# Performance work log

Hardware: AMD Instinct MI355X
Metric: run time of the kernel (lower is better)

The kernel has to match this reference:

```python
import jax, jax.numpy as jnp
import numpy as np

N, E, G, H = 5000, 50000, 8, 4
GAT_DIMS = [(1536, 1024), (1024, 512), (512, 256)]
MLP_DIMS = [(256, 128), (128, 64), (64, 32), (32, 16), (16, 1)]
GATE_DIMS = [(256, 128), (128, 1)]
NEG_SLOPE = 0.2
EPS = 1e-16


def setup_inputs() -> dict:
    key = jax.random.key(0)
    keys = iter(jax.random.split(key, 80))

    def nrm(shape, s=0.05):
        return jax.random.normal(next(keys), shape, jnp.float32) * s

    inp = {}
    inp["x"] = jax.random.normal(next(keys), (N, 1536), jnp.float32)
    inp["edge_index"] = jax.random.randint(next(keys), (2, E), 0, N)
    inp["batch"] = jnp.sort(jax.random.randint(next(keys), (N,), 0, G))
    for i, (di, do) in enumerate(GAT_DIMS, 1):
        inp[f"Wl{i}"] = nrm((di, H * do))
        inp[f"bl{i}"] = jnp.zeros((H * do,), jnp.float32)
        inp[f"Wr{i}"] = nrm((di, H * do))
        inp[f"br{i}"] = jnp.zeros((H * do,), jnp.float32)
        inp[f"att{i}"] = nrm((H, do))
        inp[f"b{i}"] = jnp.zeros((do,), jnp.float32)
    for i, (di, do) in enumerate(MLP_DIMS):
        inp[f"Wm{i}"] = nrm((di, do))
        inp[f"bm{i}"] = jnp.zeros((do,), jnp.float32)
    for i, (di, do) in enumerate(GATE_DIMS):
        inp[f"Wg{i}"] = nrm((di, do))
        inp[f"bg{i}"] = jnp.zeros((do,), jnp.float32)
    return inp


def _gatv2(x, src, dst, Wl, bl, Wr, br, att, bias):
    # PyG GATv2Conv, concat=False: mean over heads.
    C = att.shape[1]
    xl = (x @ Wl + bl).reshape(-1, H, C)  # source-side transform [N,H,C]
    xr = (x @ Wr + br).reshape(-1, H, C)  # target-side transform [N,H,C]
    # edge scores: att . leaky_relu(x_j + x_i)  -> [E',H]
    s = jnp.sum(jax.nn.leaky_relu(xl[src] + xr[dst], negative_slope=NEG_SLOPE) * att, axis=-1)
    # segment softmax over destination node neighborhoods
    m = jax.ops.segment_max(s, dst, num_segments=N)
    ex = jnp.exp(s - m[dst])
    den = jax.ops.segment_sum(ex, dst, num_segments=N)
    alpha = ex / (den[dst] + EPS)
    out = jax.ops.segment_sum(alpha[:, :, None] * xl[src], dst, num_segments=N)  # [N,H,C]
    return out.mean(axis=1) + bias


def _forward(x, edge_index, batch, params):
    loop = jnp.arange(N)
    src = jnp.concatenate([edge_index[0], loop])  # add_self_loops=True (PyG default)
    dst = jnp.concatenate([edge_index[1], loop])
    for i in (1, 2, 3):
        x = jax.nn.relu(_gatv2(x, src, dst,
                               params[f"Wl{i}"], params[f"bl{i}"],
                               params[f"Wr{i}"], params[f"br{i}"],
                               params[f"att{i}"], params[f"b{i}"]))
    # AttentionalAggregation: segment-softmax(gate_nn(x)) weighted sum over graphs
    gate = jax.nn.relu(x @ params["Wg0"] + params["bg0"]) @ params["Wg1"] + params["bg1"]
    g = gate[:, 0]
    m = jax.ops.segment_max(g, batch, num_segments=G)
    ex = jnp.exp(g - m[batch])
    den = jax.ops.segment_sum(ex, batch, num_segments=G)
    w = ex / (den[batch] + EPS)
    h = jax.ops.segment_sum(w[:, None] * x, batch, num_segments=G)  # [G,256]
    for i in range(4):
        h = jax.nn.relu(h @ params[f"Wm{i}"] + params[f"bm{i}"])
    return h @ params["Wm4"] + params["bm4"]  # [G,1]


def reference(x, edge_index, batch,
              Wl1, bl1, Wr1, br1, att1, b1,
              Wl2, bl2, Wr2, br2, att2, b2,
              Wl3, bl3, Wr3, br3, att3, b3,
              Wm0, bm0, Wm1, bm1, Wm2, bm2, Wm3, bm3, Wm4, bm4,
              Wg0, bg0, Wg1, bg1):
    params = dict(locals())
    for k in ("x", "edge_index", "batch"):
        params.pop(k)
    return _forward(x, edge_index, batch, params)
```

## Files before the change

### kernel.cpp

```cpp
#include <hip/hip_runtime.h>
#include <math.h>

#define NN 5000
#define NNP 5120
#define NE 50000
#define NEE 55000
#define NG 8
#define NH 4

typedef __attribute__((ext_vector_type(8))) _Float16 half8;
typedef __attribute__((ext_vector_type(4))) _Float16 half4;
typedef __attribute__((ext_vector_type(4))) float floatx4;


__device__ inline float waveSum(float v) {
    #pragma unroll
    for (int o = 32; o > 0; o >>= 1) v += __shfl_xor(v, o, 64);
    return v;
}
__device__ inline float waveMax(float v) {
    #pragma unroll
    for (int o = 32; o > 0; o >>= 1) v = fmaxf(v, __shfl_xor(v, o, 64));
    return v;
}

__device__ __forceinline__ void gload_lds16(const _Float16* g, _Float16* l) {
    __builtin_amdgcn_global_load_lds(
        (__attribute__((address_space(1))) void*)g,
        (__attribute__((address_space(3))) void*)l,
        16, 0, 0);
}


__global__ void k_cvtA(const float* __restrict__ X, _Float16* __restrict__ A0, int n) {
    int i = blockIdx.x * 256 + threadIdx.x;
    if (i >= n) return;
    A0[i] = (_Float16)X[i];
}

__global__ __launch_bounds__(256) void k_cvtWT(const float* __restrict__ W,
        _Float16* __restrict__ B0, int K, int M)
{
    __shared__ float tile[32][33];
    int m0 = blockIdx.x * 32, k0 = blockIdx.y * 32;
    int tx = threadIdx.x & 31, ty = threadIdx.x >> 5;
    #pragma unroll
    for (int i = 0; i < 4; ++i)
        tile[ty + 8 * i][tx] = W[(size_t)(k0 + ty + 8 * i) * M + m0 + tx];
    __syncthreads();
    #pragma unroll
    for (int i = 0; i < 4; ++i) {
        int mm = ty + 8 * i, kk = tx;
        B0[(size_t)(m0 + mm) * K + kk + k0] = (_Float16)tile[kk][mm];
    }
}

__global__ __launch_bounds__(256) void gemm_mfma_f16(
    const _Float16* __restrict__ A0, const _Float16* __restrict__ B0,
    const float* __restrict__ biasL, const float* __restrict__ biasR,
    int Nhalf, _Float16* __restrict__ C,
    int Mrows, int K, int N)
{
    __shared__ __align__(16) _Float16 smem[2 * 2 * 128 * 32];
    _Float16* As = smem;
    _Float16* Bs = smem + 2 * 128 * 32;

    const int tid = threadIdx.x;
    const int wave = tid >> 6;
    const int lane = tid & 63;
    const int wm = (wave >> 1) * 64;
    const int wn = (wave & 1) * 64;
    const int lm = lane & 15;
    const int swz = (((lane >> 4) ^ ((lane >> 1) & 3)) << 3);

    const int rowBase = blockIdx.y * 128;
    const int colBase = blockIdx.x * 128;

    floatx4 acc[4][4];
    #pragma unroll
    for (int i = 0; i < 4; ++i)
        #pragma unroll
        for (int j = 0; j < 4; ++j)
            acc[i][j] = (floatx4){0.f, 0.f, 0.f, 0.f};

    const int sr = lane >> 2;
    const int scol = (((lane & 3) ^ ((lane >> 3) & 3)) << 3);
    const _Float16* gA = A0 + (size_t)(rowBase + wave * 32 + sr) * K + scol;
    const _Float16* gB = B0 + (size_t)(colBase + wave * 32 + sr) * K + scol;
    const size_t skip16 = (size_t)16 * K;
    const int lo0 = (wave * 32) * 32;
    const int lo1 = (wave * 32 + 16) * 32;

    gload_lds16(gA, &As[lo0]);
    gload_lds16(gA + skip16, &As[lo1]);
    gload_lds16(gB, &Bs[lo0]);
    gload_lds16(gB + skip16, &Bs[lo1]);
    __syncthreads();

    const int nk = K >> 5;
    for (int t = 0; t < nk; ++t) {
        const int p = t & 1;
        const int po = p * 128 * 32;
        if (t + 1 < nk) {
            const int k1 = (t + 1) << 5;
            const int qo = (p ^ 1) * 128 * 32;
            gload_lds16(gA + k1, &As[qo + lo0]);
            gload_lds16(gA + skip16 + k1, &As[qo + lo1]);
            gload_lds16(gB + k1, &Bs[qo + lo0]);
            gload_lds16(gB + skip16 + k1, &Bs[qo + lo1]);
        }
        half8 a0[4], b0[4];
        #pragma unroll
        for (int i = 0; i < 4; ++i) {
            a0[i] = *(const half8*)&As[po + (wm + i * 16 + lm) * 32 + swz];
            b0[i] = *(const half8*)&Bs[po + (wn + i * 16 + lm) * 32 + swz];
        }
        #pragma unroll
        for (int i = 0; i < 4; ++i)
            #pragma unroll
            for (int j = 0; j < 4; ++j)
                acc[i][j] = __builtin_amdgcn_mfma_f32_16x16x32_f16(a0[i], b0[j], acc[i][j], 0, 0, 0);
        __syncthreads();
    }

    _Float16* Ct = smem;
    const int cq = (lane >> 4) * 4;
    #pragma unroll
    for (int j = 0; j < 4; ++j) {
        int col = wn + j * 16 + lm;
        int gcol = colBase + col;
        float bv = (gcol < Nhalf) ? biasL[gcol] : biasR[gcol - Nhalf];
        #pragma unroll
        for (int i = 0; i < 4; ++i) {
            int row = wm + i * 16 + cq;
            #pragma unroll
            for (int r = 0; r < 4; ++r) {
                int rr = row + r;
                Ct[rr * 128 + (col ^ (((rr >> 2) & 7) << 4))] = (_Float16)(acc[i][j][r] + bv);
            }
        }
    }
    __syncthreads();
    const int r0 = tid >> 4;
    const int cc = (tid & 15) * 8;
    #pragma unroll
    for (int ps = 0; ps < 8; ++ps) {
        int row = ps * 16 + r0;
        int grow = rowBase + row;
        if (grow < Mrows) {
            half8 v = *(const half8*)&Ct[row * 128 + (cc ^ (((row >> 2) & 7) << 4))];
            *(half8*)&C[(size_t)grow * N + colBase + cc] = v;
        }
    }
}


__global__ void k_build_edges(const int* __restrict__ ei, int* __restrict__ src,
                              int* __restrict__ dst) {
    int i = blockIdx.x * 256 + threadIdx.x;
    if (i < NE) { src[i] = ei[i]; dst[i] = ei[NE + i]; }
    else if (i < NEE) { src[i] = i - NE; dst[i] = i - NE; }
}

__global__ void k_zero32(unsigned int* __restrict__ p, int n) {
    int i = blockIdx.x * 256 + threadIdx.x;
    if (i < n) p[i] = 0u;
}

__global__ void k_count(const int* __restrict__ dst, int* __restrict__ cnt) {
    int i = blockIdx.x * 256 + threadIdx.x;
    if (i < NEE) atomicAdd(&cnt[dst[i]], 1);
}

__global__ __launch_bounds__(256) void k_scan(const int* __restrict__ cnt,
                                              int* __restrict__ off, int* __restrict__ cur) {
    __shared__ int partial[256];
    __shared__ int ppre[257];
    int t = threadIdx.x;
    const int chunk = (NN + 255) / 256;
    int lo = t * chunk, hi = min(NN, (t + 1) * chunk);
    int s = 0;
    for (int i = lo; i < hi; ++i) s += cnt[i];
    partial[t] = s;
    __syncthreads();
    if (t == 0) {
        int acc = 0;
        for (int i = 0; i < 256; ++i) { ppre[i] = acc; acc += partial[i]; }
        ppre[256] = acc;
    }
    __syncthreads();
    int acc = ppre[t];
    for (int i = lo; i < hi; ++i) { off[i] = acc; cur[i] = acc; acc += cnt[i]; }
    if (t == 0) off[NN] = ppre[256];
}

__global__ void k_fill(const int* __restrict__ src, const int* __restrict__ dst,
                       int* __restrict__ cur, int* __restrict__ slist) {
    int e = blockIdx.x * 256 + threadIdx.x;
    if (e < NEE) { int p = atomicAdd(&cur[dst[e]], 1); slist[p] = src[e]; }
}

template<int C>
__global__ __launch_bounds__(256) void k_gat_fused(
    const _Float16* __restrict__ xlr, const float* __restrict__ att,
    const int* __restrict__ eoff, const int* __restrict__ slist,
    const float* __restrict__ bias, _Float16* __restrict__ out)
{
    constexpr int LD = 2 * NH * C;
    constexpr int CH = (C >= 512) ? 8 : 4;
    constexpr int NC = C / (64 * CH);
    constexpr int PL = NC * CH;
    __shared__ float red[NH * C];
    const int n = blockIdx.x;
    const int h = threadIdx.x >> 6;
    const int lane = threadIdx.x & 63;

    float xrv[PL], attv[PL], acc[PL];
    {
        const _Float16* xrrow = xlr + (size_t)n * LD + NH * C + h * C + lane * CH;
        const float* ah = att + h * C + lane * CH;
        #pragma unroll
        for (int c = 0; c < NC; ++c) {
            if constexpr (CH == 8) {
                half8 hv = *(const half8*)(xrrow + c * 64 * CH);
                #pragma unroll
                for (int e = 0; e < 8; ++e) xrv[c * 8 + e] = (float)hv[e];
            } else {
                half4 hv = *(const half4*)(xrrow + c * 64 * CH);
                #pragma unroll
                for (int e = 0; e < 4; ++e) xrv[c * 4 + e] = (float)hv[e];
            }
            #pragma unroll
            for (int e = 0; e < CH; e += 4) {
                float4 a4 = *(const float4*)(ah + c * 64 * CH + e);
                attv[c * CH + e + 0] = a4.x; attv[c * CH + e + 1] = a4.y;
                attv[c * CH + e + 2] = a4.z; attv[c * CH + e + 3] = a4.w;
            }
        }
        #pragma unroll
        for (int e = 0; e < PL; ++e) acc[e] = 0.f;
    }

    float m = -INFINITY, den = 0.f;
    const int start = eoff[n], end = eoff[n + 1];

    _Float16 bufA[PL], bufB[PL];
    auto ldrow = [&](int s, _Float16* buf) {
        const _Float16* p = xlr + (size_t)s * LD + h * C + lane * CH;
        #pragma unroll
        for (int c = 0; c < NC; ++c) {
            if constexpr (CH == 8)
                *(half8*)&buf[c * 8] = *(const half8*)(p + c * 64 * CH);
            else
                *(half4*)&buf[c * 4] = *(const half4*)(p + c * 64 * CH);
        }
    };

    if (start < end) ldrow(slist[start], bufA);
    for (int j = start; j < end; ++j) {
        if (j + 1 < end) ldrow(slist[j + 1], bufB);
        float xv[PL];
        float ps = 0.f;
        #pragma unroll
        for (int e = 0; e < PL; ++e) {
            xv[e] = (float)bufA[e];
            float v = xv[e] + xrv[e];
            v = v > 0.f ? v : 0.2f * v;
            ps = fmaf(v, attv[e], ps);
        }
        ps = waveSum(ps);
        float m_new = fmaxf(m, ps);
        float scale = expf(m - m_new);
        float ex = expf(ps - m_new);
        den = den * scale + ex;
        m = m_new;
        #pragma unroll
        for (int e = 0; e < PL; ++e)
            acc[e] = fmaf(ex, xv[e], acc[e] * scale);
        #pragma unroll
        for (int e = 0; e < PL; ++e) bufA[e] = bufB[e];
    }

    float inv = 1.f / (den + 1e-16f);
    #pragma unroll
    for (int c = 0; c < NC; ++c) {
        int off = h * C + c * 64 * CH + lane * CH;
        #pragma unroll
        for (int e = 0; e < CH; e += 4) {
            float4 r;
            r.x = acc[c * CH + e + 0] * inv;
            r.y = acc[c * CH + e + 1] * inv;
            r.z = acc[c * CH + e + 2] * inv;
            r.w = acc[c * CH + e + 3] * inv;
            *(float4*)&red[off + e] = r;
        }
    }
    __syncthreads();

    int t = threadIdx.x;
    for (int c4 = t; c4 < C / 4; c4 += 256) {
        int c = c4 * 4;
        float4 r0 = *(const float4*)&red[0 * C + c];
        float4 r1 = *(const float4*)&red[1 * C + c];
        float4 r2 = *(const float4*)&red[2 * C + c];
        float4 r3 = *(const float4*)&red[3 * C + c];
        float4 bv = *(const float4*)(bias + c);
        half4 o;
        o[0] = (_Float16)fmaxf((r0.x + r1.x + r2.x + r3.x) * 0.25f + bv.x, 0.f);
        o[1] = (_Float16)fmaxf((r0.y + r1.y + r2.y + r3.y) * 0.25f + bv.y, 0.f);
        o[2] = (_Float16)fmaxf((r0.z + r1.z + r2.z + r3.z) * 0.25f + bv.z, 0.f);
        o[3] = (_Float16)fmaxf((r0.w + r1.w + r2.w + r3.w) * 0.25f + bv.w, 0.f);
        *(half4*)(out + (size_t)n * C + c) = o;
    }
}


__global__ __launch_bounds__(128) void k_gate(
    const _Float16* __restrict__ x, const float* __restrict__ Wg0,
    const float* __restrict__ bg0, const float* __restrict__ Wg1,
    const float* __restrict__ bg1, float* __restrict__ g)
{
    int n = blockIdx.x;
    int t = threadIdx.x;
    __shared__ float xs[256];
    __shared__ float wsum[2];
    const _Float16* xp = x + (size_t)n * 256;
    xs[t] = (float)xp[t]; xs[t + 128] = (float)xp[t + 128];
    __syncthreads();
    float acc = bg0[t];
    for (int k = 0; k < 256; ++k) acc = fmaf(xs[k], Wg0[k * 128 + t], acc);
    acc = acc > 0.f ? acc : 0.f;
    float prod = acc * Wg1[t];
    prod = waveSum(prod);
    if ((t & 63) == 0) wsum[t >> 6] = prod;
    __syncthreads();
    if (t == 0) g[n] = wsum[0] + wsum[1] + bg1[0];
}

__global__ void k_group_bounds(const int* __restrict__ batch, int* __restrict__ gstart,
                               int* __restrict__ gend) {
    int n = blockIdx.x * 256 + threadIdx.x;
    if (n >= NN) return;
    int b = batch[n];
    if (n == 0 || batch[n - 1] != b) gstart[b] = n;
    if (n == NN - 1 || batch[n + 1] != b) gend[b] = n + 1;
}

__global__ __launch_bounds__(256) void k_pool_stats(
    const float* __restrict__ g, const int* __restrict__ gstart,
    const int* __restrict__ gend, float* __restrict__ mOut,
    float* __restrict__ invdenOut)
{
    int gi = blockIdx.x;
    int t = threadIdx.x;
    int s0 = gstart[gi], e0 = gend[gi];
    __shared__ float red[4];
    float mx = -1e30f;
    for (int n = s0 + t; n < e0; n += 256) mx = fmaxf(mx, g[n]);
    float wm = waveMax(mx);
    if ((t & 63) == 0) red[t >> 6] = wm;
    __syncthreads();
    float m = fmaxf(fmaxf(red[0], red[1]), fmaxf(red[2], red[3]));
    __syncthreads();
    float sm = 0.f;
    for (int n = s0 + t; n < e0; n += 256) sm += expf(g[n] - m);
    sm = waveSum(sm);
    if ((t & 63) == 0) red[t >> 6] = sm;
    __syncthreads();
    if (t == 0) {
        float den = red[0] + red[1] + red[2] + red[3] + 1e-16f;
        mOut[gi] = m;
        invdenOut[gi] = 1.f / den;
    }
}

#define PCH 16
__global__ __launch_bounds__(256) void k_pool_acc(
    const _Float16* __restrict__ x, const float* __restrict__ g,
    const int* __restrict__ batch, const float* __restrict__ m,
    const float* __restrict__ invden, float* __restrict__ hpool)
{
    int base = blockIdx.x * PCH;
    int t = threadIdx.x;
    float acc = 0.f;
    int cur = -1;
    for (int i = 0; i < PCH; ++i) {
        int n = base + i;
        if (n >= NN) break;
        int b = batch[n];
        if (b != cur) {
            if (cur >= 0) atomicAdd(&hpool[cur * 256 + t], acc);
            cur = b; acc = 0.f;
        }
        float w = expf(g[n] - m[b]) * invden[b];
        acc = fmaf(w, (float)x[(size_t)n * 256 + t], acc);
    }
    if (cur >= 0) atomicAdd(&hpool[cur * 256 + t], acc);
}

__global__ __launch_bounds__(256) void k_mlp(
    const float* __restrict__ hpool,
    const float* __restrict__ Wm0, const float* __restrict__ bm0,
    const float* __restrict__ Wm1, const float* __restrict__ bm1,
    const float* __restrict__ Wm2, const float* __restrict__ bm2,
    const float* __restrict__ Wm3, const float* __restrict__ bm3,
    const float* __restrict__ Wm4, const float* __restrict__ bm4,
    float* __restrict__ out)
{
    __shared__ float bufA[8 * 256];
    __shared__ float bufB[8 * 128];
    int t = threadIdx.x;
    for (int i = t; i < 8 * 256; i += 256) bufA[i] = hpool[i];
    __syncthreads();
    for (int i = t; i < 8 * 128; i += 256) {
        int r = i >> 7, c = i & 127;
        float acc = bm0[c];
        for (int k = 0; k < 256; ++k) acc = fmaf(bufA[r * 256 + k], Wm0[k * 128 + c], acc);
        bufB[i] = fmaxf(acc, 0.f);
    }
    __syncthreads();
    for (int i = t; i < 8 * 64; i += 256) {
        int r = i >> 6, c = i & 63;
        float acc = bm1[c];
        for (int k = 0; k < 128; ++k) acc = fmaf(bufB[r * 128 + k], Wm1[k * 64 + c], acc);
        bufA[i] = fmaxf(acc, 0.f);
    }
    __syncthreads();
    for (int i = t; i < 8 * 32; i += 256) {
        int r = i >> 5, c = i & 31;
        float acc = bm2[c];
        for (int k = 0; k < 64; ++k) acc = fmaf(bufA[r * 64 + k], Wm2[k * 32 + c], acc);
        bufB[i] = fmaxf(acc, 0.f);
    }
    __syncthreads();
    for (int i = t; i < 8 * 16; i += 256) {
        int r = i >> 4, c = i & 15;
        float acc = bm3[c];
        for (int k = 0; k < 32; ++k) acc = fmaf(bufB[r * 32 + k], Wm3[k * 16 + c], acc);
        bufA[i] = fmaxf(acc, 0.f);
    }
    __syncthreads();
    if (t < 8) {
        float acc = bm4[0];
        for (int k = 0; k < 16; ++k) acc = fmaf(bufA[t * 16 + k], Wm4[k], acc);
        out[t] = acc;
    }
}


static void run_gat_layer(const _Float16* ain, int K, int C,
                          const float* Wl, const float* bl,
                          const float* Wr, const float* br,
                          const float* att, const float* bias,
                          _Float16* wb0, _Float16* xlr,
                          const int* eoff, const int* slist,
                          _Float16* xout, hipStream_t stream)
{
    int HC = NH * C;
    dim3 tgrid(HC / 32, K / 32);
    k_cvtWT<<<tgrid, 256, 0, stream>>>(Wl, wb0, K, HC);
    k_cvtWT<<<tgrid, 256, 0, stream>>>(Wr, wb0 + (size_t)HC * K, K, HC);
    dim3 ggrid(2 * HC / 128, NNP / 128);
    gemm_mfma_f16<<<ggrid, 256, 0, stream>>>(ain, wb0, bl, br, HC, xlr, NN, K, 2 * HC);

    if (C == 1024)
        k_gat_fused<1024><<<NN, 256, 0, stream>>>(xlr, att, eoff, slist, bias, xout);
    else if (C == 512)
        k_gat_fused<512><<<NN, 256, 0, stream>>>(xlr, att, eoff, slist, bias, xout);
    else
        k_gat_fused<256><<<NN, 256, 0, stream>>>(xlr, att, eoff, slist, bias, xout);
}

extern "C" void kernel_launch(void* const* d_in, const int* in_sizes, int n_in,
                              void* d_out, int out_size, void* d_ws, size_t ws_size,
                              hipStream_t stream) {
    const float* x      = (const float*)d_in[0];
    const int* ei       = (const int*)d_in[1];
    const int* batch    = (const int*)d_in[2];
    const float* Wl1 = (const float*)d_in[3];  const float* bl1 = (const float*)d_in[4];
    const float* Wr1 = (const float*)d_in[5];  const float* br1 = (const float*)d_in[6];
    const float* att1= (const float*)d_in[7];  const float* b1  = (const float*)d_in[8];
    const float* Wl2 = (const float*)d_in[9];  const float* bl2 = (const float*)d_in[10];
    const float* Wr2 = (const float*)d_in[11]; const float* br2 = (const float*)d_in[12];
    const float* att2= (const float*)d_in[13]; const float* b2  = (const float*)d_in[14];
    const float* Wl3 = (const float*)d_in[15]; const float* bl3 = (const float*)d_in[16];
    const float* Wr3 = (const float*)d_in[17]; const float* br3 = (const float*)d_in[18];
    const float* att3= (const float*)d_in[19]; const float* b3  = (const float*)d_in[20];
    const float* Wm0 = (const float*)d_in[21]; const float* bm0 = (const float*)d_in[22];
    const float* Wm1 = (const float*)d_in[23]; const float* bm1 = (const float*)d_in[24];
    const float* Wm2 = (const float*)d_in[25]; const float* bm2 = (const float*)d_in[26];
    const float* Wm3 = (const float*)d_in[27]; const float* bm3 = (const float*)d_in[28];
    const float* Wm4 = (const float*)d_in[29]; const float* bm4 = (const float*)d_in[30];
    const float* Wg0 = (const float*)d_in[31]; const float* bg0 = (const float*)d_in[32];
    const float* Wg1 = (const float*)d_in[33]; const float* bg1 = (const float*)d_in[34];
    float* out = (float*)d_out;

    float* ws = (float*)d_ws;
    size_t o = 0;
    _Float16* xlr = (_Float16*)(ws + o); o += (size_t)NNP * 8192 / 2;
    _Float16* x1  = (_Float16*)(ws + o); o += (size_t)NNP * 1024 / 2;
    _Float16* x2  = (_Float16*)(ws + o); o += (size_t)NNP * 512 / 2;
    _Float16* x3  = (_Float16*)(ws + o); o += (size_t)NNP * 256 / 2;
    _Float16* a0p = (_Float16*)(ws + o); o += (size_t)NNP * 1536 / 2;
    _Float16* wb0 = (_Float16*)(ws + o); o += (size_t)8192 * 1536 / 2;
    int* srcA    = (int*)(ws + o); o += NEE;
    int* dstA    = (int*)(ws + o); o += NEE;
    int* cnt     = (int*)(ws + o); o += NN;
    int* eoff    = (int*)(ws + o); o += NN + 1;
    int* cur     = (int*)(ws + o); o += NN;
    int* slist   = (int*)(ws + o); o += NEE;
    float* g     = ws + o; o += NN;
    int* gstart  = (int*)(ws + o); o += NG;
    int* gend    = (int*)(ws + o); o += NG;
    float* gm    = ws + o; o += NG;
    float* ginv  = ws + o; o += NG;
    float* hpool = ws + o; o += NG * 256;

    int ebB = (NEE + 255) / 256;
    k_build_edges<<<ebB, 256, 0, stream>>>(ei, srcA, dstA);
    k_zero32<<<(NN + 255) / 256, 256, 0, stream>>>((unsigned int*)cnt, NN);
    k_count<<<ebB, 256, 0, stream>>>(dstA, cnt);
    k_scan<<<1, 256, 0, stream>>>(cnt, eoff, cur);
    k_fill<<<ebB, 256, 0, stream>>>(srcA, dstA, cur, slist);

    int nA = NN * 1536;
    k_cvtA<<<(nA + 255) / 256, 256, 0, stream>>>(x, a0p, nA);

    run_gat_layer(a0p, 1536, 1024, Wl1, bl1, Wr1, br1, att1, b1,
                  wb0, xlr, eoff, slist, x1, stream);
    run_gat_layer(x1,  1024, 512,  Wl2, bl2, Wr2, br2, att2, b2,
                  wb0, xlr, eoff, slist, x2, stream);
    run_gat_layer(x2,  512,  256,  Wl3, bl3, Wr3, br3, att3, b3,
                  wb0, xlr, eoff, slist, x3, stream);

    k_gate<<<NN, 128, 0, stream>>>(x3, Wg0, bg0, Wg1, bg1, g);
    k_zero32<<<1, 64, 0, stream>>>((unsigned int*)gstart, 2 * NG);
    k_group_bounds<<<(NN + 255) / 256, 256, 0, stream>>>(batch, gstart, gend);
    k_pool_stats<<<NG, 256, 0, stream>>>(g, gstart, gend, gm, ginv);
    k_zero32<<<(NG * 256 + 255) / 256, 256, 0, stream>>>((unsigned int*)hpool, NG * 256);
    k_pool_acc<<<(NN + PCH - 1) / PCH, 256, 0, stream>>>(x3, g, batch, gm, ginv, hpool);
    k_mlp<<<1, 256, 0, stream>>>(hpool, Wm0, bm0, Wm1, bm1, Wm2, bm2,
                                 Wm3, bm3, Wm4, bm4, out);
}
```

Before: 699.7 us.

## Add 256x256-tile 8-wave MFMA GEMM with ping-pong staged loads for large layers

Adds a new GEMM kernel that uses 256x256 output tiles, 512 threads and a double-buffered LDS pipeline. Each K-step is split into four quadrant phases that interleave async global-to-LDS loads with MFMA work, using explicit vmcnt waits, barriers and priority raising. It is used for the two larger GAT layers (C>=512) in place of the 128x128 kernel, aiming for more operand reuse and better overlap of memory with compute. The cost is heavier register and LDS use and fewer blocks in flight. The fragile waitcnt accounting is a correctness risk.

```diff
diff --git a/kernel.cpp b/kernel.cpp
--- a/kernel.cpp
+++ b/kernel.cpp
@@ -31,6 +31,13 @@
         16, 0, 0);
 }
 
+template<int N>
+__device__ __forceinline__ void vmgate() {
+    if constexpr (N == 0) asm volatile("s_waitcnt vmcnt(0)" ::: "memory");
+    else if constexpr (N == 2) asm volatile("s_waitcnt vmcnt(2)" ::: "memory");
+    else if constexpr (N == 4) asm volatile("s_waitcnt vmcnt(4)" ::: "memory");
+}
+
 
 __global__ void k_cvtA(const float* __restrict__ X, _Float16* __restrict__ A0, int n) {
     int i = blockIdx.x * 256 + threadIdx.x;
@@ -52,6 +59,166 @@
     for (int i = 0; i < 4; ++i) {
         int mm = ty + 8 * i, kk = tx;
         B0[(size_t)(m0 + mm) * K + kk + k0] = (_Float16)tile[kk][mm];
+    }
+}
+
+__global__ __launch_bounds__(512, 2) void gemm256_mfma_f16(
+    const _Float16* __restrict__ A0, const _Float16* __restrict__ B0,
+    const float* __restrict__ biasL, const float* __restrict__ biasR,
+    int Nhalf, _Float16* __restrict__ C,
+    int Mrows, int K, int N)
+{
+    __shared__ __align__(16) _Float16 smem[2 * 32768];
+
+    const int tid  = threadIdx.x;
+    const int wave = tid >> 6;
+    const int lane = tid & 63;
+    const int wr = wave >> 2;
+    const int wc = wave & 3;
+    const int rowBase = blockIdx.y * 256;
+    const int colBase = blockIdx.x * 256;
+
+    floatx4 acc[2][2][4][2];
+    #pragma unroll
+    for (int qa = 0; qa < 2; ++qa)
+        #pragma unroll
+        for (int qb = 0; qb < 2; ++qb)
+            #pragma unroll
+            for (int f = 0; f < 4; ++f)
+                #pragma unroll
+                for (int g = 0; g < 2; ++g)
+                    acc[qa][qb][f][g] = (floatx4){0.f, 0.f, 0.f, 0.f};
+
+    const int srow   = lane >> 3;
+    const int schunk = ((lane & 7) ^ srow) << 3;
+    const _Float16* gA = A0 + (size_t)(rowBase + wave * 16 + srow) * K + schunk;
+    const _Float16* gB = B0 + (size_t)(colBase + wave * 16 + srow) * K + schunk;
+    const size_t rstep = (size_t)8 * K;
+    const size_t hstep = (size_t)128 * K;
+
+    auto stageA = [&](int b, int h, int kt) {
+        _Float16* l = &smem[b * 32768 + (h * 128 + wave * 16) * 64];
+        const _Float16* g = gA + (size_t)h * hstep + (size_t)kt * 64;
+        gload_lds16(g, l);
+        gload_lds16(g + rstep, l + 512);
+    };
+    auto stageB = [&](int b, int h, int kt) {
+        _Float16* l = &smem[b * 32768 + 16384 + (h * 128 + wave * 16) * 64];
+        const _Float16* g = gB + (size_t)h * hstep + (size_t)kt * 64;
+        gload_lds16(g, l);
+        gload_lds16(g + rstep, l + 512);
+    };
+
+    auto phase = [&](auto qa_c, auto qb_c, auto gate_c, const _Float16* Ab,
+                     const _Float16* Bb, auto stg) {
+        constexpr int QA = decltype(qa_c)::value;
+        constexpr int QB = decltype(qb_c)::value;
+        constexpr int GATE = decltype(gate_c)::value;
+        const int lm = lane & 15;
+        const int key = lane & 7;
+        const int kg = lane >> 4;
+        half8 af[4][2], bf[2][2];
+        #pragma unroll
+        for (int f = 0; f < 4; ++f)
+            #pragma unroll
+            for (int s = 0; s < 2; ++s) {
+                int row = QA * 128 + wr * 64 + f * 16 + lm;
+                int ch = (s * 4 + kg) ^ key;
+                af[f][s] = *(const half8*)&Ab[row * 64 + ch * 8];
+            }
+        #pragma unroll
+        for (int g = 0; g < 2; ++g)
+            #pragma unroll
+            for (int s = 0; s < 2; ++s) {
+                int row = QB * 128 + wc * 32 + g * 16 + lm;
+                int ch = (s * 4 + kg) ^ key;
+                bf[g][s] = *(const half8*)&Bb[row * 64 + ch * 8];
+            }
+        stg();
+        __builtin_amdgcn_s_barrier();
+        __builtin_amdgcn_s_setprio(1);
+        #pragma unroll
+        for (int f = 0; f < 4; ++f)
+            #pragma unroll
+            for (int g = 0; g < 2; ++g)
+                #pragma unroll
+                for (int s = 0; s < 2; ++s)
+                    acc[QA][QB][f][g] = __builtin_amdgcn_mfma_f32_16x16x32_f16(
+                        af[f][s], bf[g][s], acc[QA][QB][f][g], 0, 0, 0);
+        __builtin_amdgcn_s_setprio(0);
+        vmgate<GATE>();
+        __builtin_amdgcn_s_barrier();
+        __builtin_amdgcn_sched_barrier(0);
+    };
+
+    auto ic = [](auto v) { return v; };
+    using i0 = std::integral_constant<int, 0>;
+    using i1 = std::integral_constant<int, 1>;
+    using gN = std::integral_constant<int, -1>;
+    using g0 = std::integral_constant<int, 0>;
+    using g2 = std::integral_constant<int, 2>;
+    using g4 = std::integral_constant<int, 4>;
+    (void)ic;
+
+    stageA(0, 0, 0); stageA(0, 1, 0); stageB(0, 0, 0); stageB(0, 1, 0);
+    vmgate<2>();
+    __builtin_amdgcn_s_barrier();
+
+    const int nk = K >> 6;
+    for (int t = 0; t < nk - 1; ++t) {
+        const int b = t & 1;
+        const _Float16* Ab = &smem[b * 32768];
+        const _Float16* Bb = Ab + 16384;
+        phase(i0{}, i0{}, gN{}, Ab, Bb, [&]{ stageA(b ^ 1, 0, t + 1); });
+        phase(i1{}, i0{}, g4{}, Ab, Bb, [&]{ stageA(b ^ 1, 1, t + 1); });
+        phase(i0{}, i1{}, gN{}, Ab, Bb, [&]{ stageB(b ^ 1, 0, t + 1); });
+        phase(i1{}, i1{}, g2{}, Ab, Bb, [&]{ stageB(b ^ 1, 1, t + 1); });
+    }
+    {
+        const int b = (nk - 1) & 1;
+        const _Float16* Ab = &smem[b * 32768];
+        const _Float16* Bb = Ab + 16384;
+        phase(i0{}, i0{}, gN{}, Ab, Bb, [&]{});
+        phase(i1{}, i0{}, g0{}, Ab, Bb, [&]{});
+        phase(i0{}, i1{}, gN{}, Ab, Bb, [&]{});
+        phase(i1{}, i1{}, gN{}, Ab, Bb, [&]{});
+    }
+
+    _Float16* Ct = smem;
+    const int lm = lane & 15;
+    const int cq = (lane >> 4) * 4;
+    #pragma unroll
+    for (int qb = 0; qb < 2; ++qb)
+        #pragma unroll
+        for (int g = 0; g < 2; ++g) {
+            int col = qb * 128 + wc * 32 + g * 16 + lm;
+            int gcol = colBase + col;
+            float bv = (gcol < Nhalf) ? biasL[gcol] : biasR[gcol - Nhalf];
+            #pragma unroll
+            for (int qa = 0; qa < 2; ++qa)
+                #pragma unroll
+                for (int f = 0; f < 4; ++f)
+                    #pragma unroll
+                    for (int r = 0; r < 4; ++r) {
+                        int row = qa * 128 + wr * 64 + f * 16 + cq + r;
+                        int gi = (col >> 4) ^ ((row >> 2) & 7);
+                        Ct[row * 256 + gi * 16 + (col & 15)] =
+                            (_Float16)(acc[qa][qb][f][g][r] + bv);
+                    }
+        }
+    __syncthreads();
+    const int r0 = tid >> 5;
+    const int cc = (tid & 31) * 8;
+    const int gg = cc >> 4;
+    #pragma unroll
+    for (int ps = 0; ps < 16; ++ps) {
+        int row = ps * 16 + r0;
+        int grow = rowBase + row;
+        if (grow < Mrows) {
+            int gp = gg ^ ((row >> 2) & 7);
+            half8 v = *(const half8*)&Ct[row * 256 + gp * 16 + (cc & 15)];
+            *(half8*)&C[(size_t)grow * N + colBase + cc] = v;
+        }
     }
 }
 
@@ -460,8 +627,13 @@
     dim3 tgrid(HC / 32, K / 32);
     k_cvtWT<<<tgrid, 256, 0, stream>>>(Wl, wb0, K, HC);
     k_cvtWT<<<tgrid, 256, 0, stream>>>(Wr, wb0 + (size_t)HC * K, K, HC);
-    dim3 ggrid(2 * HC / 128, NNP / 128);
-    gemm_mfma_f16<<<ggrid, 256, 0, stream>>>(ain, wb0, bl, br, HC, xlr, NN, K, 2 * HC);
+    if (C >= 512) {
+        dim3 ggrid(2 * HC / 256, NNP / 256);
+        gemm256_mfma_f16<<<ggrid, 512, 0, stream>>>(ain, wb0, bl, br, HC, xlr, NN, K, 2 * HC);
+    } else {
+        dim3 ggrid(2 * HC / 128, NNP / 128);
+        gemm_mfma_f16<<<ggrid, 256, 0, stream>>>(ain, wb0, bl, br, HC, xlr, NN, K, 2 * HC);
+    }
 
     if (C == 1024)
         k_gat_fused<1024><<<NN, 256, 0, stream>>>(xlr, att, eoff, slist, bias, xout);
```

After: 695.6 us. About the same (-0.6%).
